# Kernel optimization log

Hardware: AMD Instinct MI355X
Metric: run time of the kernel (lower is better)

The kernel has to match this reference:

```python
import jax, jax.numpy as jnp
import numpy as np

DELTA = 6.0      # 3 / (1 - alpha), alpha = 0.5
ETA = 1.0
MS_ITER = 3
D_FEAT = 256
N_PTS = 8192
X_SCALE = 0.06   # keeps ||x||^2 ~ 0.9 so exp(DELTA * X^T X) is well-conditioned


def setup_inputs() -> dict:
    key = jax.random.key(0)
    X = jax.random.normal(key, (D_FEAT, N_PTS), dtype=jnp.float32) * X_SCALE
    return {"X": X}


def _mean_shift_once(X):
    # X: [d, N]
    S = jnp.einsum('dn,dm->nm', X, X)          # X^T X, [N, N]
    K = jnp.exp(DELTA * S)                     # Gaussian-like affinity, [N, N]
    colsum = jnp.sum(K, axis=0)                # d = K^T @ ones  -> column sums, [N]
    # X @ P with P = (1-eta) I + eta K D_inv; D_inv = diag(1/colsum).
    # X @ K @ D_inv == (X @ K) / colsum (per-column scaling) -- no diag/eye materialized.
    XK = X @ K                                 # [d, N]
    return (1.0 - ETA) * X + ETA * (XK / colsum[None, :])


def reference(X):
    outs = []
    cur = X
    for _ in range(MS_ITER):
        cur = _mean_shift_once(cur)
        outs.append(cur)
    return tuple(outs)
```

## Files before the change

kernel.cpp:

```cpp
#include <hip/hip_runtime.h>
#include <hip/hip_bf16.h>
#include <stdint.h>

#define DFEAT 256
#define NPTS  8192

typedef __attribute__((ext_vector_type(8)))  short bf16x8;
typedef __attribute__((ext_vector_type(16))) float f32x16;
typedef __attribute__((ext_vector_type(4)))  int   int4v;
typedef __attribute__((ext_vector_type(4)))  float f32x4;

#define AS1 __attribute__((address_space(1)))
#define AS3 __attribute__((address_space(3)))

__device__ inline void dma16(const void* g, void* l) {
  __builtin_amdgcn_global_load_lds((const AS1 uint32_t*)g, (AS3 uint32_t*)l, 16, 0, 0);
}

__device__ inline uint16_t f2bf(float f) {
  union { float f; uint32_t u; } v; v.f = f;
  return (uint16_t)((v.u + 0x7FFFu + ((v.u >> 16) & 1u)) >> 16);
}


__global__ __launch_bounds__(256, 2) void ms_fused(
    const uint16_t* __restrict__ xaf,
    const uint16_t* __restrict__ xbf,
    float* __restrict__ num,
    float* __restrict__ cs)
{
  __shared__ __attribute__((aligned(16))) uint16_t XT[2][16384];
  __shared__ __attribute__((aligned(16))) uint16_t Ps[64 * 64];

  const int tid  = threadIdx.x;
  const int w    = tid >> 6;
  const int lane = tid & 63;
  const int l31  = lane & 31;
  const int g    = lane >> 5;
  const int mt   = blockIdx.x & 127;
  const int q    = blockIdx.x >> 7;
  const int m0   = mt * 64;
  const int a_sub = w >> 1;
  const int b_sub = w & 1;

  const char* xafc = (const char*)xaf;
  const char* xbfc = (const char*)xbf;
  char*       Psc  = (char*)Ps;

  bf16x8 Bm[16];
  {
    const char* bp = xafc + (size_t)(m0 / 32 + b_sub) * 16384 + g * 512 + l31 * 16;
    #pragma unroll
    for (int ks = 0; ks < 16; ++ks)
      Bm[ks] = __builtin_bit_cast(bf16x8, *(const int4v*)(bp + ks * 1024));
  }

  f32x16 accO[2][2];
  #pragma unroll
  for (int i = 0; i < 2; ++i)
    #pragma unroll
    for (int j = 0; j < 2; ++j)
      #pragma unroll
      for (int r = 0; r < 16; ++r) accO[i][j][r] = 0.0f;
  float csacc = 0.0f;

  const int mloc = 32 * b_sub + l31;
  const int l7   = l31 & 7;
  const int j0   = q * 32;

  {
    const char* src = xafc + (size_t)j0 * 32768;
    #pragma unroll
    for (int r = 0; r < 8; ++r)
      dma16(src + tid * 16 + r * 4096, (char*)XT[0] + tid * 16 + r * 4096);
  }

  for (int t = 0; t < 32; ++t) {
    const int jt  = j0 + t;
    const int cur = t & 1;
    __syncthreads();

    if (t < 31) {
      const char* src = xafc + (size_t)(jt + 1) * 32768;
      #pragma unroll
      for (int r = 0; r < 8; ++r)
        dma16(src + tid * 16 + r * 4096,
              (char*)XT[cur ^ 1] + tid * 16 + r * 4096);
    }

    const int n0 = jt * 64;
    bf16x8 Xf[2][4];
    #pragma unroll
    for (int t2 = 0; t2 < 2; ++t2) {
      const char* xp = xbfc + (size_t)(2 * w + t2) * 524288 +
                       (size_t)(n0 >> 3) * 512 + g * 512 + l31 * 16;
      #pragma unroll
      for (int ks = 0; ks < 4; ++ks)
        Xf[t2][ks] = __builtin_bit_cast(bf16x8, *(const int4v*)(xp + ks * 1024));
    }

    f32x16 s;
    #pragma unroll
    for (int r = 0; r < 16; ++r) s[r] = 0.0f;
    {
      const char* ap = (const char*)XT[cur] + a_sub * 16384 + g * 512 + l31 * 16;
      #pragma unroll
      for (int ks = 0; ks < 16; ++ks) {
        bf16x8 A = __builtin_bit_cast(bf16x8, *(const int4v*)(ap + ks * 1024));
        s = __builtin_amdgcn_mfma_f32_32x32x16_bf16(A, Bm[ks], s, 0, 0, 0);
      }
    }

    #pragma unroll
    for (int k = 0; k < 4; ++k) {
      float e0 = __expf(6.0f * s[4*k+0]);
      float e1 = __expf(6.0f * s[4*k+1]);
      float e2 = __expf(6.0f * s[4*k+2]);
      float e3 = __expf(6.0f * s[4*k+3]);
      csacc += (e0 + e1) + (e2 + e3);
      uint32_t lo = (uint32_t)f2bf(e0) | ((uint32_t)f2bf(e1) << 16);
      uint32_t hi = (uint32_t)f2bf(e2) | ((uint32_t)f2bf(e3) << 16);
      int p = (4 * a_sub + k) ^ (mloc & 7);
      *(uint64_t*)(Psc + mloc * 128 + p * 16 + 8 * g) =
          ((uint64_t)hi << 32) | lo;
    }
    __syncthreads();

    #pragma unroll
    for (int ks = 0; ks < 4; ++ks) {
      bf16x8 Bp[2];
      #pragma unroll
      for (int mm = 0; mm < 2; ++mm) {
        int mrow = 32 * mm + l31;
        int p = (2 * ks + g) ^ l7;
        Bp[mm] = __builtin_bit_cast(bf16x8,
            *(const int4v*)(Psc + mrow * 128 + p * 16));
      }
      #pragma unroll
      for (int t2 = 0; t2 < 2; ++t2) {
        accO[t2][0] = __builtin_amdgcn_mfma_f32_32x32x16_bf16(Xf[t2][ks], Bp[0], accO[t2][0], 0,0,0);
        accO[t2][1] = __builtin_amdgcn_mfma_f32_32x32x16_bf16(Xf[t2][ks], Bp[1], accO[t2][1], 0,0,0);
      }
    }
  }

  csacc += __shfl_xor(csacc, 32, 64);
  if (g == 0) atomicAdd(&cs[m0 + mloc], csacc);
  #pragma unroll
  for (int t2 = 0; t2 < 2; ++t2)
    #pragma unroll
    for (int mm = 0; mm < 2; ++mm)
      #pragma unroll
      for (int r = 0; r < 16; ++r) {
        int drow = 32 * (2 * w + t2) + (r & 3) + 8 * (r >> 2) + 4 * g;
        int mg   = m0 + 32 * mm + l31;
        atomicAdd(&num[(size_t)drow * NPTS + mg], accO[t2][mm][r]);
      }
}

__global__ __launch_bounds__(256) void ms_combine(
    const float* __restrict__ src, const float* __restrict__ csr,
    float* __restrict__ csz, float* __restrict__ yout,
    float* __restrict__ numz,
    uint16_t* __restrict__ xaf, uint16_t* __restrict__ xbf,
    const int mode)
{
  __shared__ uint16_t T[64][66];
  const int tid = threadIdx.x;
  const int n0 = blockIdx.x * 64;
  const int d0 = blockIdx.y * 64;

  #pragma unroll
  for (int i = 0; i < 4; ++i) {
    int e  = tid + i * 256;
    int dl = e >> 4, nq = e & 15;
    size_t idx = (size_t)(d0 + dl) * NPTS + (n0 + nq * 4);
    f32x4 v = *(const f32x4*)(src + idx);
    if (mode) {
      f32x4 c = *(const f32x4*)(csr + n0 + nq * 4);
      v /= c;
      *(f32x4*)(yout + idx) = v;
      f32x4 z = {0.f, 0.f, 0.f, 0.f};
      *(f32x4*)(numz + idx) = z;
    }
    #pragma unroll
    for (int k = 0; k < 4; ++k) T[dl][nq * 4 + k] = f2bf(v[k]);
  }
  if (mode && blockIdx.y == 0 && tid < 64) csz[n0 + tid] = 0.0f;
  __syncthreads();

  char* xafc = (char*)xaf;
  char* xbfc = (char*)xbf;
  #pragma unroll
  for (int i = 0; i < 2; ++i) {
    int c  = tid + i * 256;
    int nb = c >> 8, s2 = (c >> 5) & 7, ln = c & 31;
    union { uint32_t u[4]; int4v v; } pk;
    #pragma unroll
    for (int k = 0; k < 4; ++k) {
      uint32_t lo = T[s2 * 8 + 2 * k][nb * 32 + ln];
      uint32_t hi = T[s2 * 8 + 2 * k + 1][nb * 32 + ln];
      pk.u[k] = lo | (hi << 16);
    }
    *(int4v*)(xafc + (size_t)(n0 / 32 + nb) * 16384 +
              (size_t)(d0 / 8 + s2) * 512 + ln * 16) = pk.v;
  }
  #pragma unroll
  for (int i = 0; i < 2; ++i) {
    int c  = tid + i * 256;
    int db = c >> 8, uu = (c >> 5) & 7, ln = c & 31;
    const uint16_t* tr = &T[db * 32 + ln][uu * 8];
    union { uint32_t u[4]; int4v v; } pk;
    #pragma unroll
    for (int k = 0; k < 4; ++k)
      pk.u[k] = (uint32_t)tr[2 * k] | ((uint32_t)tr[2 * k + 1] << 16);
    *(int4v*)(xbfc + (size_t)(d0 / 32 + db) * 524288 +
              (size_t)(n0 / 8 + uu) * 512 + ln * 16) = pk.v;
  }
}

extern "C" void kernel_launch(void* const* d_in, const int* in_sizes, int n_in,
                              void* d_out, int out_size, void* d_ws, size_t ws_size,
                              hipStream_t stream)
{
  (void)in_sizes; (void)n_in; (void)out_size; (void)ws_size;
  const float* X = (const float*)d_in[0];
  float* out = (float*)d_out;
  char* ws = (char*)d_ws;
  uint16_t* xaf = (uint16_t*)(ws);
  uint16_t* xbf = (uint16_t*)(ws + (4u << 20));
  float*    num = (float*)   (ws + (8u << 20));
  float*    cs0 = (float*)   (ws + (16u << 20));
  float*    cs1 = (float*)   (ws + (16u << 20) + 32768);

  hipMemsetAsync(ws + (8u << 20), 0, (8u << 20) + 65536, stream);

  dim3 cgrid(NPTS / 64, DFEAT / 64);
  ms_combine<<<cgrid, 256, 0, stream>>>(X, nullptr, nullptr, nullptr, nullptr,
                                        xaf, xbf, 0);
  for (int it = 0; it < 3; ++it) {
    float* csA = (it & 1) ? cs1 : cs0;
    float* csB = (it & 1) ? cs0 : cs1;
    ms_fused<<<512, 256, 0, stream>>>(xaf, xbf, num, csA);
    ms_combine<<<cgrid, 256, 0, stream>>>(num, csA, csB,
                                          out + (size_t)it * DFEAT * NPTS,
                                          num, xaf, xbf, 1);
  }
}
```

Baseline: 347.8 us.

## Single-buffer XT tile and raise fused-kernel occupancy to three blocks per CU

```diff
diff --git a/kernel.cpp b/kernel.cpp
--- a/kernel.cpp
+++ b/kernel.cpp
@@ -23,13 +23,13 @@
 }
 
 
-__global__ __launch_bounds__(256, 2) void ms_fused(
+__global__ __launch_bounds__(256, 3) void ms_fused(
     const uint16_t* __restrict__ xaf,
     const uint16_t* __restrict__ xbf,
     float* __restrict__ num,
     float* __restrict__ cs)
 {
-  __shared__ __attribute__((aligned(16))) uint16_t XT[2][16384];
+  __shared__ __attribute__((aligned(16))) uint16_t XT[16384];
   __shared__ __attribute__((aligned(16))) uint16_t Ps[64 * 64];
 
   const int tid  = threadIdx.x;
@@ -43,6 +43,9 @@
   const int a_sub = w >> 1;
   const int b_sub = w & 1;
 
+  const int nt = 21 + (q < 2 ? 1 : 0);
+  const int j0 = q * 21 + (q < 2 ? q : 2);
+
   const char* xafc = (const char*)xaf;
   const char* xbfc = (const char*)xbf;
   char*       Psc  = (char*)Ps;
@@ -66,49 +69,40 @@
 
   const int mloc = 32 * b_sub + l31;
   const int l7   = l31 & 7;
-  const int j0   = q * 32;
 
   {
     const char* src = xafc + (size_t)j0 * 32768;
     #pragma unroll
     for (int r = 0; r < 8; ++r)
-      dma16(src + tid * 16 + r * 4096, (char*)XT[0] + tid * 16 + r * 4096);
-  }
-
-  for (int t = 0; t < 32; ++t) {
-    const int jt  = j0 + t;
-    const int cur = t & 1;
-    __syncthreads();
-
-    if (t < 31) {
-      const char* src = xafc + (size_t)(jt + 1) * 32768;
-      #pragma unroll
-      for (int r = 0; r < 8; ++r)
-        dma16(src + tid * 16 + r * 4096,
-              (char*)XT[cur ^ 1] + tid * 16 + r * 4096);
-    }
-
-    const int n0 = jt * 64;
-    bf16x8 Xf[2][4];
-    #pragma unroll
-    for (int t2 = 0; t2 < 2; ++t2) {
-      const char* xp = xbfc + (size_t)(2 * w + t2) * 524288 +
-                       (size_t)(n0 >> 3) * 512 + g * 512 + l31 * 16;
-      #pragma unroll
-      for (int ks = 0; ks < 4; ++ks)
-        Xf[t2][ks] = __builtin_bit_cast(bf16x8, *(const int4v*)(xp + ks * 1024));
-    }
+      dma16(src + tid * 16 + r * 4096, (char*)XT + tid * 16 + r * 4096);
+  }
+  __syncthreads();
+
+  for (int t = 0; t < nt; ++t) {
+    const int jt = j0 + t;
 
     f32x16 s;
     #pragma unroll
     for (int r = 0; r < 16; ++r) s[r] = 0.0f;
     {
-      const char* ap = (const char*)XT[cur] + a_sub * 16384 + g * 512 + l31 * 16;
+      const char* ap = (const char*)XT + a_sub * 16384 + g * 512 + l31 * 16;
       #pragma unroll
       for (int ks = 0; ks < 16; ++ks) {
         bf16x8 A = __builtin_bit_cast(bf16x8, *(const int4v*)(ap + ks * 1024));
         s = __builtin_amdgcn_mfma_f32_32x32x16_bf16(A, Bm[ks], s, 0, 0, 0);
       }
+    }
+
+    const int n0 = jt * 64;
+    const char* xp0 = xbfc + (size_t)(2 * w + 0) * 524288 +
+                      (size_t)(n0 >> 3) * 512 + g * 512 + l31 * 16;
+    const char* xp1 = xbfc + (size_t)(2 * w + 1) * 524288 +
+                      (size_t)(n0 >> 3) * 512 + g * 512 + l31 * 16;
+    bf16x8 Xf01[2][2];
+    #pragma unroll
+    for (int ks = 0; ks < 2; ++ks) {
+      Xf01[0][ks] = __builtin_bit_cast(bf16x8, *(const int4v*)(xp0 + ks * 1024));
+      Xf01[1][ks] = __builtin_bit_cast(bf16x8, *(const int4v*)(xp1 + ks * 1024));
     }
 
     #pragma unroll
@@ -124,7 +118,22 @@
       *(uint64_t*)(Psc + mloc * 128 + p * 16 + 8 * g) =
           ((uint64_t)hi << 32) | lo;
     }
+
     __syncthreads();
+
+    bf16x8 Xf23[2][2];
+    #pragma unroll
+    for (int ks = 0; ks < 2; ++ks) {
+      Xf23[0][ks] = __builtin_bit_cast(bf16x8, *(const int4v*)(xp0 + (ks+2) * 1024));
+      Xf23[1][ks] = __builtin_bit_cast(bf16x8, *(const int4v*)(xp1 + (ks+2) * 1024));
+    }
+
+    if (t < nt - 1) {
+      const char* src = xafc + (size_t)(jt + 1) * 32768;
+      #pragma unroll
+      for (int r = 0; r < 8; ++r)
+        dma16(src + tid * 16 + r * 4096, (char*)XT + tid * 16 + r * 4096);
+    }
 
     #pragma unroll
     for (int ks = 0; ks < 4; ++ks) {
@@ -138,10 +147,13 @@
       }
       #pragma unroll
       for (int t2 = 0; t2 < 2; ++t2) {
-        accO[t2][0] = __builtin_amdgcn_mfma_f32_32x32x16_bf16(Xf[t2][ks], Bp[0], accO[t2][0], 0,0,0);
-        accO[t2][1] = __builtin_amdgcn_mfma_f32_32x32x16_bf16(Xf[t2][ks], Bp[1], accO[t2][1], 0,0,0);
-      }
-    }
+        bf16x8 Af = (ks < 2) ? Xf01[t2][ks] : Xf23[t2][ks - 2];
+        accO[t2][0] = __builtin_amdgcn_mfma_f32_32x32x16_bf16(Af, Bp[0], accO[t2][0], 0,0,0);
+        accO[t2][1] = __builtin_amdgcn_mfma_f32_32x32x16_bf16(Af, Bp[1], accO[t2][1], 0,0,0);
+      }
+    }
+
+    __syncthreads();
   }
 
   csacc += __shfl_xor(csacc, 32, 64);
@@ -241,7 +253,7 @@
   for (int it = 0; it < 3; ++it) {
     float* csA = (it & 1) ? cs1 : cs0;
     float* csB = (it & 1) ? cs0 : cs1;
-    ms_fused<<<512, 256, 0, stream>>>(xaf, xbf, num, csA);
+    ms_fused<<<768, 256, 0, stream>>>(xaf, xbf, num, csA);
     ms_combine<<<cgrid, 256, 0, stream>>>(num, csA, csB,
                                           out + (size_t)it * DFEAT * NPTS,
                                           num, xaf, xbf, 1);
```

New measurement: 448.8 us. 29.0% more time.
